# Performance work log

Measured on AMD Instinct MI355X. Metric: run time of the kernel, lower is better.

The kernel has to match this reference:

```python
import jax, jax.numpy as jnp
import numpy as np

B, N, L = 16, 128, 512            # batch, scan length, per-step feature (= configs.seq_len)
D, S, K, R, H = 1024, 16, 4, 64, 2048  # d_model, d_state, ker_size, dt_rank, hidden_dimention


def _mamba_params(key, scale=0.02):
    ks = jax.random.split(key, 6)
    return dict(
        in_w=jax.random.normal(ks[0], (2 * D, L)) * scale,
        conv_w=jax.random.normal(ks[1], (D, K)) * scale,
        conv_b=jnp.zeros((D,)),
        xproj_w=jax.random.normal(ks[2], (R + 2 * S, D)) * scale,
        dt_w=jax.random.normal(ks[3], (D, R)) * scale,
        dt_b=jax.random.normal(ks[4], (D,)) * scale,
        A_log=jnp.tile(jnp.log(jnp.arange(1, S + 1, dtype=jnp.float32)), (D, 1)),
        Dp=jnp.ones((D,)),
        out_w=jax.random.normal(ks[5], (L, D)) * scale,
    )


def setup_inputs():
    key = jax.random.key(0)
    kx, kf, kr, k1, k2 = jax.random.split(key, 5)
    inp = {"x": jax.random.normal(kx, (B, N, L), dtype=jnp.float32)}
    for pre, k in (("f_", kf), ("r_", kr)):
        for n, v in _mamba_params(k).items():
            inp[pre + n] = v
    inp["pu_w"] = jax.random.normal(k1, (H, L)) * 0.02
    inp["pu_b"] = jnp.zeros((H,))
    inp["pl_w"] = jax.random.normal(k2, (L, H)) * 0.02
    inp["pl_b"] = jnp.zeros((L,))
    inp["ln_g"] = jnp.ones((L,))
    inp["ln_b"] = jnp.zeros((L,))
    return inp


def _ln(x, g, b, eps=1e-5):
    m = x.mean(-1, keepdims=True)
    v = ((x - m) ** 2).mean(-1, keepdims=True)
    return (x - m) * jax.lax.rsqrt(v + eps) * g + b


def _dw_causal_conv(x, w, b):
    # x: [B,N,D]; depthwise causal conv along N with kernel [D,K]
    xt = jnp.pad(x.transpose(0, 2, 1), ((0, 0), (0, 0), (K - 1, 0)))  # [B,D,N+K-1]
    y = jax.lax.conv_general_dilated(xt, w[:, None, :], (1,), 'VALID',
                                     dimension_numbers=('NCH', 'OIH', 'NCH'),
                                     feature_group_count=D)
    return (y + b[None, :, None]).transpose(0, 2, 1)


def _mamba(x, in_w, conv_w, conv_b, xproj_w, dt_w, dt_b, A_log, Dp, out_w):
    # standard Mamba block (in_proj -> depthwise conv -> silu -> selective scan -> gate -> out_proj)
    xi, res = jnp.split(x @ in_w.T, 2, axis=-1)             # [B,N,D] each
    xc = jax.nn.silu(_dw_causal_conv(xi, conv_w, conv_b))   # [B,N,D]
    dbc = xc @ xproj_w.T                                    # [B,N,R+2S]
    dt, Bm, Cm = dbc[..., :R], dbc[..., R:R + S], dbc[..., R + S:]
    delta = jax.nn.softplus(dt @ dt_w.T + dt_b)             # [B,N,D]
    A = -jnp.exp(A_log)                                     # [D,S]
    dA = jnp.exp(delta[..., None] * A)                      # [B,N,D,S]
    dBx = delta[..., None] * Bm[:, :, None, :] * xc[..., None]

    def step(h, t):
        dA_t, dBx_t, C_t = t
        h = dA_t * h + dBx_t                                # [B,D,S]
        return h, jnp.einsum('bds,bs->bd', h, C_t)

    _, ys = jax.lax.scan(step, jnp.zeros((x.shape[0], D, S), x.dtype),
                         (dA.transpose(1, 0, 2, 3), dBx.transpose(1, 0, 2, 3), Cm.transpose(1, 0, 2)))
    y = ys.transpose(1, 0, 2) + xc * Dp                     # [B,N,D]
    y = y * jax.nn.silu(res)
    return y @ out_w.T                                      # [B,N,L]


def reference(x, f_in_w, f_conv_w, f_conv_b, f_xproj_w, f_dt_w, f_dt_b, f_A_log, f_Dp, f_out_w,
              r_in_w, r_conv_w, r_conv_b, r_xproj_w, r_dt_w, r_dt_b, r_A_log, r_Dp, r_out_w,
              pu_w, pu_b, pl_w, pl_b, ln_g, ln_b):
    y1 = _mamba(x, f_in_w, f_conv_w, f_conv_b, f_xproj_w, f_dt_w, f_dt_b, f_A_log, f_Dp, f_out_w)
    y2 = _mamba(x[:, ::-1, :], r_in_w, r_conv_w, r_conv_b, r_xproj_w, r_dt_w, r_dt_b, r_A_log, r_Dp, r_out_w)
    y3 = _ln(x + y1 + y2[:, ::-1, :], ln_g, ln_b)
    yp = jax.nn.relu(y3 @ pu_w.T + pu_b)
    yp = yp @ pl_w.T + pl_b
    return _ln(yp + y3, ln_g, ln_b)
```

## Files before the change

### kernel.cpp

```cpp
#include <hip/hip_runtime.h>
#include <hip/hip_bf16.h>
#include <cstdint>

typedef __hip_bfloat16 bf16;

constexpr int Bb = 16, Nn = 128, Ll = 512, Dd = 1024, Ss = 16, Rr = 64, Hh = 2048;
constexpr int Mm = Bb * Nn;
#define LOG2E 1.44269504088896340736f

using bf16x8 = __attribute__((ext_vector_type(8))) __bf16;
using bf16x4 = __attribute__((ext_vector_type(4))) __bf16;
using f32x4  = __attribute__((ext_vector_type(4))) float;

__device__ __forceinline__ float to_f(float x) { return x; }
__device__ __forceinline__ float to_f(bf16 x) { return __bfloat162float(x); }
__device__ __forceinline__ void store_t(float* p, float v) { *p = v; }
__device__ __forceinline__ void store_t(bf16* p, float v) { *p = __float2bfloat16(v); }
__device__ __forceinline__ __bf16 cvt1(float x) {
  bf16 h = __float2bfloat16(x);
  return *reinterpret_cast<__bf16*>(&h);
}
__device__ __forceinline__ float bfraw_to_f(__bf16 x) {
  bf16 h = *reinterpret_cast<bf16*>(&x);
  return __bfloat162float(h);
}
__device__ __forceinline__ bf16x8 load8(const bf16* p) { return *(const bf16x8*)p; }
__device__ __forceinline__ bf16x8 load8(const float* p) {
  float4 a = *(const float4*)p;
  float4 b = *(const float4*)(p + 4);
  bf16x8 r;
  r[0] = cvt1(a.x); r[1] = cvt1(a.y); r[2] = cvt1(a.z); r[3] = cvt1(a.w);
  r[4] = cvt1(b.x); r[5] = cvt1(b.y); r[6] = cvt1(b.z); r[7] = cvt1(b.w);
  return r;
}
__device__ __forceinline__ bf16x8 load8rt(const void* p, size_t idx, int isbf) {
  if (isbf) return load8((const bf16*)p + idx);
  return load8((const float*)p + idx);
}
__device__ __forceinline__ float ldf(const void* p, int i, int isbf) {
  if (isbf) return __bfloat162float(((const bf16*)p)[i]);
  return ((const float*)p)[i];
}
__device__ __forceinline__ void gld16(const bf16* g, __bf16* l) {
  __builtin_amdgcn_global_load_lds(
      (const __attribute__((address_space(1))) void*)g,
      (__attribute__((address_space(3))) void*)l, 16, 0, 0);
}
#if __has_builtin(__builtin_amdgcn_mov_dpp)
__device__ __forceinline__ float quad_xor1(float v) {
  int r = __builtin_amdgcn_mov_dpp(__builtin_bit_cast(int, v), 0xB1, 0xF, 0xF, true);
  return __builtin_bit_cast(float, r);
}
__device__ __forceinline__ float quad_xor2(float v) {
  int r = __builtin_amdgcn_mov_dpp(__builtin_bit_cast(int, v), 0x4E, 0xF, 0xF, true);
  return __builtin_bit_cast(float, r);
}
#else
__device__ __forceinline__ float quad_xor1(float v) { return __shfl_xor(v, 1, 64); }
__device__ __forceinline__ float quad_xor2(float v) { return __shfl_xor(v, 2, 64); }
#endif

enum { EPI_STORE = 0, EPI_BIAS_RELU = 1, EPI_ADD = 3, EPI_BIAS = 4, EPI_BIAS_SOFTPLUS = 5,
       EPI_ATOMIC = 6 };

__global__ void sniff_kernel(const unsigned short* __restrict__ xs, int* __restrict__ flags) {
  const int tid = threadIdx.x;
  int cnt = 0;
  for (int j = 0; j < 64; ++j) {
    int i = tid + j * 256;
    unsigned short u = xs[(size_t)i * 64];
    bf16 h = *reinterpret_cast<bf16*>(&u);
    float v = __bfloat162float(h);
    float a = fabsf(v);
    if (v == 0.f || (a > 0.0009765625f && a < 16.f)) ++cnt;
  }
  __shared__ int sc[256];
  sc[tid] = cnt;
  __syncthreads();
  for (int o = 128; o > 0; o >>= 1) {
    if (tid < o) sc[tid] += sc[tid + o];
    __syncthreads();
  }
  if (tid == 0) flags[0] = (sc[0] > 8192) ? 1 : 0;
}

__global__ __launch_bounds__(256) void prep_kernel(
    const int* __restrict__ flagp, const void* __restrict__ x,
    float* __restrict__ ZB, unsigned short* __restrict__ Xb,
    float* __restrict__ zerop,
    const void* __restrict__ fin, const void* __restrict__ rin,
    const void* __restrict__ fout, const void* __restrict__ rout,
    const void* __restrict__ puw, const void* __restrict__ plw,
    bf16* __restrict__ WBin, bf16* __restrict__ WBout,
    bf16* __restrict__ WBpu, bf16* __restrict__ WBpl) {
  const int isbf = *flagp;
  const int i = blockIdx.x * 256 + threadIdx.x;
  if (i < 262144) {
    float4 o;
    ushort4 u;
    if (isbf) {
      u = ((const ushort4*)x)[i];
      bf16 h0 = *reinterpret_cast<bf16*>(&u.x), h1 = *reinterpret_cast<bf16*>(&u.y);
      bf16 h2 = *reinterpret_cast<bf16*>(&u.z), h3 = *reinterpret_cast<bf16*>(&u.w);
      o = float4{__bfloat162float(h0), __bfloat162float(h1),
                 __bfloat162float(h2), __bfloat162float(h3)};
    } else {
      o = ((const float4*)x)[i];
      bf16 h0 = __float2bfloat16(o.x), h1 = __float2bfloat16(o.y);
      bf16 h2 = __float2bfloat16(o.z), h3 = __float2bfloat16(o.w);
      u = ushort4{*(unsigned short*)&h0, *(unsigned short*)&h1,
                  *(unsigned short*)&h2, *(unsigned short*)&h3};
    }
    ((float4*)ZB)[i] = o;
    ((ushort4*)Xb)[i] = u;
  } else if (i < 622592) {
    ((float4*)zerop)[i - 262144] = float4{0.f, 0.f, 0.f, 0.f};
  } else {
    const int j = i - 622592;
    const void* src;
    bf16* dst;
    int si;
    if (j < 131072) { src = fin; si = j; dst = WBin + (size_t)si * 8; }
    else if (j < 262144) { src = rin; si = j - 131072; dst = WBin + (size_t)1048576 + (size_t)si * 8; }
    else if (j < 393216) { src = puw; si = j - 262144; dst = WBpu + (size_t)si * 8; }
    else if (j < 524288) { src = plw; si = j - 393216; dst = WBpl + (size_t)si * 8; }
    else if (j < 589824) {
      src = fout; si = j - 524288;
      int e = si * 8;
      dst = WBout + (size_t)(e >> 10) * 2048 + (e & 1023);
    } else {
      src = rout; si = j - 589824;
      int e = si * 8;
      dst = WBout + (size_t)(e >> 10) * 2048 + 1024 + (e & 1023);
    }
    *(bf16x8*)dst = load8rt(src, (size_t)si * 8, isbf);
  }
}

constexpr int LDT2 = 72;

template <typename TC, int EPI>
__global__ __launch_bounds__(256) void gemm_rt(
    const int* __restrict__ flagp,
    const void* __restrict__ A, int lda, int abf,
    const void* __restrict__ Bw, const void* __restrict__ Bw2, int ldb,
    int bmode, int bsplit,
    TC* __restrict__ C, int ldc,
    const void* __restrict__ bias, const void* __restrict__ bias2,
    int N, int Kchunk, int zk, size_t a_doff, size_t c_doff) {
  const int isbf = *flagp;
  const int ab = (abf == 2) ? isbf : abf;
  __shared__ __align__(16) __bf16 As[64 * LDT2];
  __shared__ __align__(16) __bf16 Bs[64 * LDT2];
  const int tid = threadIdx.x;
  const int wave = tid >> 6, lane = tid & 63;
  const int quad = lane >> 4, l16 = lane & 15;
  const int wm = wave & 1, wn = wave >> 1;
  int bx = blockIdx.x, by = blockIdx.y;
  const int gx = gridDim.x, gy = gridDim.y;
  if ((gx & 7) == 0) {
    int id = bx + gx * by;
    int xcd = id & 7, sl = id >> 3;
    by = sl % gy;
    bx = (sl / gy) * 8 + xcd;
  }
  int zsl = blockIdx.z;
  const void* Ap = A;
  const void* Bp0 = Bw;
  const void* biasp = bias;
  if (bmode == 3) {
    const int dir = zsl / zk;
    zsl = zsl % zk;
    if (dir) {
      Ap = (const char*)A + a_doff * (size_t)(ab ? 2 : 4);
      C += c_doff;
      Bp0 = Bw2;
      biasp = bias2;
    }
  }
  const int m0 = by * 64, n0 = bx * 64;
  const int kb = zsl * Kchunk;
  const int srow = tid >> 3;
  const int scol = (tid & 7) * 8;
  f32x4 acc[2][2] = {};
  for (int k0 = kb; k0 < kb + Kchunk; k0 += 64) {
#pragma unroll
    for (int h = 0; h < 2; ++h) {
      int r = srow + h * 32;
      *(bf16x8*)(&As[r * LDT2 + scol]) =
          load8rt(Ap, (size_t)(m0 + r) * lda + k0 + scol, ab);
      int rb = n0 + r;
      rb = rb < N ? rb : N - 1;
      size_t bi = (size_t)rb * ldb + k0 + scol;
      *(bf16x8*)(&Bs[r * LDT2 + scol]) = load8rt(Bp0, bi, isbf);
    }
    __syncthreads();
#pragma unroll
    for (int kk2 = 0; kk2 < 2; ++kk2) {
      bf16x8 af[2], bfr[2];
#pragma unroll
      for (int i = 0; i < 2; ++i)
        af[i] = *(const bf16x8*)(&As[(wm * 32 + i * 16 + l16) * LDT2 + kk2 * 32 + quad * 8]);
#pragma unroll
      for (int j = 0; j < 2; ++j)
        bfr[j] = *(const bf16x8*)(&Bs[(wn * 32 + j * 16 + l16) * LDT2 + kk2 * 32 + quad * 8]);
#pragma unroll
      for (int i = 0; i < 2; ++i)
#pragma unroll
        for (int j = 0; j < 2; ++j)
          acc[i][j] = __builtin_amdgcn_mfma_f32_16x16x32_bf16(af[i], bfr[j], acc[i][j], 0, 0, 0);
    }
    __syncthreads();
  }
#pragma unroll
  for (int i = 0; i < 2; ++i) {
#pragma unroll
    for (int j = 0; j < 2; ++j) {
      const int col = n0 + wn * 32 + j * 16 + l16;
      if (col >= N) continue;
      float bv = 0.f;
      if (EPI == EPI_BIAS_RELU || EPI == EPI_BIAS || EPI == EPI_BIAS_SOFTPLUS)
        bv = ldf(biasp, col, isbf);
#pragma unroll
      for (int r = 0; r < 4; ++r) {
        const int row = m0 + wm * 32 + i * 16 + quad * 4 + r;
        size_t idx = (size_t)row * ldc + col;
        float v = acc[i][j][r];
        if (EPI == EPI_STORE) store_t(&C[idx], v);
        else if (EPI == EPI_BIAS_RELU) { v += bv; store_t(&C[idx], v > 0.f ? v : 0.f); }
        else if (EPI == EPI_BIAS) store_t(&C[idx], v + bv);
        else if (EPI == EPI_BIAS_SOFTPLUS) {
          v += bv;
          store_t(&C[idx], (v > 20.f) ? v : log1pf(__expf(v)));
        } else if (EPI == EPI_ATOMIC) {
          atomicAdd((float*)&C[idx], v);
        }
      }
    }
  }
}

template <typename TC, int EPI>
__global__ __launch_bounds__(256) void gemm128n(
    const int* __restrict__ flagp,
    const bf16* __restrict__ A, int lda,
    const bf16* __restrict__ Bw, int ldb,
    TC* __restrict__ C, int ldc,
    const void* __restrict__ bias,
    int Kchunk) {
  __shared__ __align__(16) __bf16 As[2][128 * 64];
  __shared__ __align__(16) __bf16 Bs[2][128 * 64];
  const int tid = threadIdx.x;
  const int wave = tid >> 6, lane = tid & 63;
  const int quad = lane >> 4, l16 = lane & 15;
  const int wr = wave >> 1, wc = wave & 1;
  int bx = blockIdx.x, by = blockIdx.y;
  const int gx = gridDim.x, gy = gridDim.y;
  if ((gx & 7) == 0) {
    int id = bx + gx * by;
    int xcd = id & 7, sl = id >> 3;
    by = sl % gy;
    bx = (sl / gy) * 8 + xcd;
  }
  const int m0 = by * 128, n0 = bx * 128;
  const int kb = blockIdx.z * Kchunk;
  const int kend = kb + Kchunk;
  const int lr = lane >> 3;
  const int lc = (lane & 7) * 8;
  auto STAGE = [&](int buf, int k0) {
#pragma unroll
    for (int rr = 0; rr < 4; ++rr) {
      const int rowb = rr * 32 + wave * 8;
      gld16(A + (size_t)(m0 + rowb + lr) * lda + k0 + lc, &As[buf][rowb * 64]);
      gld16(Bw + (size_t)(n0 + rowb + lr) * ldb + k0 + lc, &Bs[buf][rowb * 64]);
    }
  };
  f32x4 acc[4][4] = {};
  int cur = 0;
  STAGE(0, kb);
  __syncthreads();
  for (int k0 = kb; k0 < kend; k0 += 64) {
    if (k0 + 64 < kend) STAGE(cur ^ 1, k0 + 64);
#pragma unroll
    for (int kk = 0; kk < 2; ++kk) {
      bf16x8 af[4], bfr[4];
#pragma unroll
      for (int i = 0; i < 4; ++i)
        af[i] = *(const bf16x8*)(&As[cur][(wr * 64 + i * 16 + l16) * 64 + kk * 32 + quad * 8]);
#pragma unroll
      for (int j = 0; j < 4; ++j)
        bfr[j] = *(const bf16x8*)(&Bs[cur][(wc * 64 + j * 16 + l16) * 64 + kk * 32 + quad * 8]);
#pragma unroll
      for (int i = 0; i < 4; ++i)
#pragma unroll
        for (int j = 0; j < 4; ++j)
          acc[i][j] = __builtin_amdgcn_mfma_f32_16x16x32_bf16(af[i], bfr[j], acc[i][j], 0, 0, 0);
    }
    __syncthreads();
    cur ^= 1;
  }
  const int isbf = *flagp;
#pragma unroll
  for (int i = 0; i < 4; ++i) {
#pragma unroll
    for (int j = 0; j < 4; ++j) {
      const int col = n0 + wc * 64 + j * 16 + l16;
      float bv = 0.f;
      if (EPI == EPI_BIAS_RELU) bv = ldf(bias, col, isbf);
#pragma unroll
      for (int r = 0; r < 4; ++r) {
        const int row = m0 + wr * 64 + i * 16 + quad * 4 + r;
        size_t idx = (size_t)row * ldc + col;
        float v = acc[i][j][r];
        if (EPI == EPI_STORE) store_t(&C[idx], v);
        else if (EPI == EPI_BIAS_RELU) { v += bv; store_t(&C[idx], v > 0.f ? v : 0.f); }
        else if (EPI == EPI_ATOMIC) atomicAdd((float*)&C[idx], v);
      }
    }
  }
}

__global__ __launch_bounds__(256) void conv_silu_rt(
    const int* __restrict__ flagp, const bf16* __restrict__ X2b,
    const void* __restrict__ fcw, const void* __restrict__ fcb,
    const void* __restrict__ rcw, const void* __restrict__ rcb,
    bf16* __restrict__ XCb) {
  const int isbf = *flagp;
  const int dir = blockIdx.y >> 2;
  const int d = (blockIdx.y & 3) * 256 + threadIdx.x;
  const int m = blockIdx.x;
  const int t = m & (Nn - 1);
  const void* cw = dir ? rcw : fcw;
  const void* cb = dir ? rcb : fcb;
  float w0 = ldf(cw, d * 4 + 0, isbf), w1 = ldf(cw, d * 4 + 1, isbf);
  float w2 = ldf(cw, d * 4 + 2, isbf), w3 = ldf(cw, d * 4 + 3, isbf);
  float a = ldf(cb, d, isbf);
  const size_t base = (size_t)m * 4096 + (size_t)dir * 2048 + d;
  if (dir == 0) {
    if (t >= 3) a += w0 * to_f(X2b[base - 3 * 4096]);
    if (t >= 2) a += w1 * to_f(X2b[base - 2 * 4096]);
    if (t >= 1) a += w2 * to_f(X2b[base - 1 * 4096]);
    a += w3 * to_f(X2b[base]);
  } else {
    if (t + 3 < Nn) a += w0 * to_f(X2b[base + 3 * 4096]);
    if (t + 2 < Nn) a += w1 * to_f(X2b[base + 2 * 4096]);
    if (t + 1 < Nn) a += w2 * to_f(X2b[base + 1 * 4096]);
    a += w3 * to_f(X2b[base]);
  }
  const float s = a / (1.f + __builtin_amdgcn_exp2f(-a * LOG2E));
  XCb[(size_t)m * 2048 + (size_t)dir * 1024 + d] = __float2bfloat16(s);
}

__global__ __launch_bounds__(256) void scan_gate8(
    const int* __restrict__ flagp,
    const float* __restrict__ DBC0, bf16* __restrict__ XCb, const bf16* __restrict__ X2b,
    const bf16* __restrict__ DELTA0,
    const void* __restrict__ fAlog, const void* __restrict__ fDp,
    const void* __restrict__ rAlog, const void* __restrict__ rDp) {
  const int isbf = *flagp;
  const int dir = blockIdx.z;
  const float* DBC = DBC0 + (size_t)dir * Mm * 96;
  const bf16* DELTA = DELTA0 + (size_t)dir * Mm * 1024;
  const void* A_log = dir ? rAlog : fAlog;
  const void* Dp = dir ? rDp : fDp;
  __shared__ __align__(16) __bf16 sBC[Nn * 32];
  __shared__ __align__(16) __bf16 sD[Nn * 64];
  __shared__ __align__(16) __bf16 sX[Nn * 64];
  __shared__ __align__(16) __bf16 sG[Nn * 64];
  __shared__ __align__(16) __bf16 sY[Nn * 64];
  const int b = blockIdx.x;
  const int d0 = blockIdx.y * 64;
  const int tid = threadIdx.x;
  const size_t rowbase = (size_t)b * Nn;
  const size_t xc_col = (size_t)dir * 1024;
#pragma unroll
  for (int k = 0; k < 4; ++k) {
    int idx = tid + k * 256;
    int t = idx >> 3, c = idx & 7;
    float4 v = *(const float4*)(DBC + (rowbase + t) * 96 + 64 + c * 4);
    bf16x4 pv = {cvt1(v.x), cvt1(v.y), cvt1(v.z), cvt1(v.w)};
    int dst = (c < 4) ? (t * 32 + c * 8) : (t * 32 + (c - 4) * 8 + 4);
    *(bf16x4*)&sBC[dst] = pv;
  }
#pragma unroll
  for (int k = 0; k < 4; ++k) {
    int idx = tid + k * 256;
    int t = idx >> 3, h = idx & 7;
    *(uint4*)&sD[t * 64 + h * 8] =
        *(const uint4*)(DELTA + (rowbase + t) * 1024 + d0 + h * 8);
    *(uint4*)&sX[t * 64 + h * 8] =
        *(const uint4*)(XCb + (rowbase + t) * 2048 + xc_col + d0 + h * 8);
    bf16x8 rv = *(const bf16x8*)(X2b + (rowbase + t) * 4096 + (size_t)dir * 2048 + 1024 + d0 + h * 8);
    bf16x8 gv;
#pragma unroll
    for (int e = 0; e < 8; ++e) {
      float r = bfraw_to_f(rv[e]);
      gv[e] = cvt1(r / (1.f + __builtin_amdgcn_exp2f(-r * LOG2E)));
    }
    *(bf16x8*)&sG[t * 64 + h * 8] = gv;
  }
  __syncthreads();
  const int wv = tid >> 6, lane = tid & 63;
  const int sg = lane & 3, dl = lane >> 2;
  const int d_local = wv * 16 + dl;
  const int d = d0 + d_local;
  float A_[4];
#pragma unroll
  for (int j = 0; j < 4; ++j)
    A_[j] = -__expf(ldf(A_log, d * Ss + sg * 4 + j, isbf)) * LOG2E;
  const float dp = ldf(Dp, d, isbf);
  float h0 = 0.f, h1 = 0.f, h2 = 0.f, h3 = 0.f;
  for (int pg = 0; pg < Nn / 4; ++pg) {
    float accs[4], xvs[4];
#pragma unroll
    for (int u = 0; u < 4; ++u) {
      const int p = pg * 4 + u;
      const int t = dir ? (Nn - 1 - p) : p;
      const float dv = bfraw_to_f(sD[t * 64 + d_local]);
      const float xv = bfraw_to_f(sX[t * 64 + d_local]);
      bf16x8 bc = *(const bf16x8*)&sBC[t * 32 + sg * 8];
      const float dx = dv * xv;
      h0 = __builtin_amdgcn_exp2f(dv * A_[0]) * h0 + dx * bfraw_to_f(bc[0]);
      h1 = __builtin_amdgcn_exp2f(dv * A_[1]) * h1 + dx * bfraw_to_f(bc[1]);
      h2 = __builtin_amdgcn_exp2f(dv * A_[2]) * h2 + dx * bfraw_to_f(bc[2]);
      h3 = __builtin_amdgcn_exp2f(dv * A_[3]) * h3 + dx * bfraw_to_f(bc[3]);
      accs[u] = h0 * bfraw_to_f(bc[4]) + h1 * bfraw_to_f(bc[5]) +
                h2 * bfraw_to_f(bc[6]) + h3 * bfraw_to_f(bc[7]);
      xvs[u] = xv;
    }
#pragma unroll
    for (int u = 0; u < 4; ++u) {
      float a = accs[u];
      a += quad_xor1(a);
      a += quad_xor2(a);
      if (sg == 0) {
        const int p = pg * 4 + u;
        const int t = dir ? (Nn - 1 - p) : p;
        const float g = bfraw_to_f(sG[t * 64 + d_local]);
        sY[t * 64 + d_local] = cvt1((a + xvs[u] * dp) * g);
      }
    }
  }
  __syncthreads();
#pragma unroll
  for (int k = 0; k < 4; ++k) {
    int idx = tid + k * 256;
    int t = idx >> 3, h = idx & 7;
    *(uint4*)(XCb + (rowbase + t) * 2048 + xc_col + d0 + h * 8) =
        *(const uint4*)&sY[t * 64 + h * 8];
  }
}

template <int MODE>
__global__ __launch_bounds__(256) void ln_rt(const int* __restrict__ flagp,
                                             const float* __restrict__ Z,
                                             const float* __restrict__ Zadd,
                                             const void* __restrict__ g,
                                             const void* __restrict__ bb,
                                             const void* __restrict__ pb,
                                             void* __restrict__ outp,
                                             bf16* __restrict__ outp2) {
  const int isbf = *flagp;
  const int row = blockIdx.x;
  const int tid = threadIdx.x;
  const int c0 = tid * 2;
  const float2* z = (const float2*)(Z + (size_t)row * Ll);
  float2 v = z[tid];
  if (MODE == 1) {
    const float2* za = (const float2*)(Zadd + (size_t)row * Ll);
    float2 a = za[tid];
    v.x += a.x + ldf(pb, c0, isbf);
    v.y += a.y + ldf(pb, c0 + 1, isbf);
  }
  float s = v.x + v.y, q = v.x * v.x + v.y * v.y;
#pragma unroll
  for (int o = 32; o > 0; o >>= 1) {
    s += __shfl_xor(s, o, 64);
    q += __shfl_xor(q, o, 64);
  }
  __shared__ float ss[4], qq[4];
  const int wv = tid >> 6, ln = tid & 63;
  if (ln == 0) { ss[wv] = s; qq[wv] = q; }
  __syncthreads();
  s = ss[0] + ss[1] + ss[2] + ss[3];
  q = qq[0] + qq[1] + qq[2] + qq[3];
  const float mean = s * (1.f / Ll);
  const float var = q * (1.f / Ll) - mean * mean;
  const float rs = rsqrtf(var + 1e-5f);
  const float o0 = (v.x - mean) * rs * ldf(g, c0, isbf) + ldf(bb, c0, isbf);
  const float o1 = (v.y - mean) * rs * ldf(g, c0 + 1, isbf) + ldf(bb, c0 + 1, isbf);
  if (MODE == 0) {
    float* out = (float*)outp;
    out[(size_t)row * Ll + c0] = o0;
    out[(size_t)row * Ll + c0 + 1] = o1;
    outp2[(size_t)row * Ll + c0] = __float2bfloat16(o0);
    outp2[(size_t)row * Ll + c0 + 1] = __float2bfloat16(o1);
  } else {
    if (isbf) {
      bf16* out = (bf16*)outp;
      out[(size_t)row * Ll + c0] = __float2bfloat16(o0);
      out[(size_t)row * Ll + c0 + 1] = __float2bfloat16(o1);
    } else {
      float* out = (float*)outp;
      out[(size_t)row * Ll + c0] = o0;
      out[(size_t)row * Ll + c0 + 1] = o1;
    }
  }
}

extern "C" void kernel_launch(void* const* d_in, const int* in_sizes, int n_in, void* d_out,
                              int out_size, void* d_ws, size_t ws_size, hipStream_t stream) {
  char* ws = (char*)d_ws;
  int* flags = (int*)ws;
  bf16* X2b = (bf16*)(ws + 256);
  bf16* XCb = X2b + (size_t)Mm * 4096;
  bf16* Y3b = XCb + (size_t)Mm * 2048;
  bf16* DELTA = Y3b + (size_t)Mm * 512;
  bf16* Xb = DELTA + (size_t)2 * Mm * 1024;
  bf16* WBin = Xb + (size_t)Mm * 512;
  bf16* WBout = WBin + (size_t)4096 * 512;
  bf16* WBpu = WBout + (size_t)512 * 2048;
  bf16* WBpl = WBpu + (size_t)2048 * 512;
  float* DBC = (float*)(WBpl + (size_t)512 * 2048);
  float* Z2 = DBC + (size_t)2 * Mm * 96;
  float* ZB = Z2 + (size_t)Mm * 512;
  float* Y3 = ZB + (size_t)Mm * 512;
  bf16* H1 = X2b;
  size_t needed = 256 +
                  2 * ((size_t)Mm * 4096 + (size_t)Mm * 2048 + (size_t)Mm * 512 +
                       (size_t)2 * Mm * 1024 + (size_t)Mm * 512 +
                       (size_t)4096 * 512 + (size_t)512 * 2048 +
                       (size_t)2048 * 512 + (size_t)512 * 2048) +
                  4 * ((size_t)2 * Mm * 96 + (size_t)3 * Mm * 512);
  if (ws_size < needed) return;

  const void* x = d_in[0];
  const dim3 blk(256);

  sniff_kernel<<<dim3(1), blk, 0, stream>>>((const unsigned short*)x, flags);
  prep_kernel<<<dim3(4992), blk, 0, stream>>>(
      flags, x, ZB, (unsigned short*)Xb, DBC,
      d_in[1], d_in[10], d_in[9], d_in[18], d_in[19], d_in[21],
      WBin, WBout, WBpu, WBpl);
  gemm128n<bf16, EPI_STORE><<<dim3(32, 16), blk, 0, stream>>>(
      flags, Xb, Ll, WBin, Ll, X2b, 4096, nullptr, Ll);
  conv_silu_rt<<<dim3(Mm, 8), blk, 0, stream>>>(flags, X2b, d_in[2], d_in[3],
                                                d_in[11], d_in[12], XCb);
  gemm_rt<float, EPI_ATOMIC><<<dim3(2, 32, 8), blk, 0, stream>>>(
      flags, XCb, 2048, 1, d_in[4], d_in[13], Dd, 3, 0,
      DBC, 96, nullptr, nullptr, 96, 256, 4, 1024, (size_t)Mm * 96);
  gemm_rt<bf16, EPI_BIAS_SOFTPLUS><<<dim3(16, 32, 2), blk, 0, stream>>>(
      flags, DBC, 96, 0, d_in[5], d_in[14], Rr, 3, 0,
      DELTA, 1024, d_in[6], d_in[15], 1024, Rr, 1, (size_t)Mm * 96, (size_t)Mm * 1024);
  scan_gate8<<<dim3(Bb, Dd / 64, 2), blk, 0, stream>>>(
      flags, DBC, XCb, X2b, DELTA, d_in[7], d_in[8], d_in[16], d_in[17]);
  gemm128n<float, EPI_ATOMIC><<<dim3(4, 16, 4), blk, 0, stream>>>(
      flags, XCb, 2048, WBout, 2048, ZB, Ll, nullptr, Ll);
  ln_rt<0><<<dim3(Mm), blk, 0, stream>>>(flags, ZB, nullptr, d_in[23], d_in[24], nullptr,
                                         (void*)Y3, Y3b);
  gemm128n<bf16, EPI_BIAS_RELU><<<dim3(16, 16), blk, 0, stream>>>(
      flags, Y3b, Ll, WBpu, Ll, H1, Hh, d_in[20], Ll);
  gemm128n<float, EPI_ATOMIC><<<dim3(4, 16, 4), blk, 0, stream>>>(
      flags, H1, Hh, WBpl, 2048, Z2, Ll, nullptr, Ll);
  ln_rt<1><<<dim3(Mm), blk, 0, stream>>>(flags, Z2, Y3, d_in[23], d_in[24], d_in[22],
                                         d_out, nullptr);

  (void)in_sizes; (void)n_in; (void)out_size;
}
```

Measured before the change: 314.2 us.

## Fuse dt projection and softplus into scan kernel via MFMA

Removes the separate dt-projection GEMM launch and the DELTA global buffer. Each scan block now computes its 128x64 delta tile in place with MFMA, reading the DBC dt columns and dt weights, then applies bias and softplus into shared memory. The gate and output tiles reuse the staging shared memory to keep the LDS footprint the same. This saves a launch and the DELTA write and read, at the cost of extra per-block compute and an added sync phase in front of the scan.

Result: no change. 312.4 us (median of 2 runs) (-0.6%).

```diff
diff --git a/kernel.cpp b/kernel.cpp
--- a/kernel.cpp
+++ b/kernel.cpp
@@ -351,28 +351,43 @@
   XCb[(size_t)m * 2048 + (size_t)dir * 1024 + d] = __float2bfloat16(s);
 }
 
-__global__ __launch_bounds__(256) void scan_gate8(
+__global__ __launch_bounds__(256) void scan_gate9(
     const int* __restrict__ flagp,
     const float* __restrict__ DBC0, bf16* __restrict__ XCb, const bf16* __restrict__ X2b,
-    const bf16* __restrict__ DELTA0,
+    const void* __restrict__ fdtw, const void* __restrict__ fdtb,
+    const void* __restrict__ rdtw, const void* __restrict__ rdtb,
     const void* __restrict__ fAlog, const void* __restrict__ fDp,
     const void* __restrict__ rAlog, const void* __restrict__ rDp) {
   const int isbf = *flagp;
   const int dir = blockIdx.z;
   const float* DBC = DBC0 + (size_t)dir * Mm * 96;
-  const bf16* DELTA = DELTA0 + (size_t)dir * Mm * 1024;
+  const void* dtw = dir ? rdtw : fdtw;
+  const void* dtb = dir ? rdtb : fdtb;
   const void* A_log = dir ? rAlog : fAlog;
   const void* Dp = dir ? rDp : fDp;
   __shared__ __align__(16) __bf16 sBC[Nn * 32];
   __shared__ __align__(16) __bf16 sD[Nn * 64];
   __shared__ __align__(16) __bf16 sX[Nn * 64];
-  __shared__ __align__(16) __bf16 sG[Nn * 64];
-  __shared__ __align__(16) __bf16 sY[Nn * 64];
+  __shared__ __align__(16) __bf16 uni[2 * Nn * 64];
+  __bf16* At = uni;
+  __bf16* Bt = uni + 128 * LDT2;
+  __bf16* sG = uni;
+  __bf16* sY = uni + Nn * 64;
   const int b = blockIdx.x;
   const int d0 = blockIdx.y * 64;
   const int tid = threadIdx.x;
   const size_t rowbase = (size_t)b * Nn;
   const size_t xc_col = (size_t)dir * 1024;
+  const int wave = tid >> 6, lane = tid & 63;
+  const int quad = lane >> 4, l16 = lane & 15;
+#pragma unroll
+  for (int k = 0; k < 8; ++k) {
+    int idx = tid + k * 256;
+    int t = idx >> 4, c4 = (idx & 15) * 4;
+    float4 v = *(const float4*)(DBC + (rowbase + t) * 96 + c4);
+    bf16x4 pv = {cvt1(v.x), cvt1(v.y), cvt1(v.z), cvt1(v.w)};
+    *(bf16x4*)&At[t * LDT2 + c4] = pv;
+  }
 #pragma unroll
   for (int k = 0; k < 4; ++k) {
     int idx = tid + k * 256;
@@ -383,13 +398,57 @@
     *(bf16x4*)&sBC[dst] = pv;
   }
 #pragma unroll
+  for (int k = 0; k < 2; ++k) {
+    int c8 = tid + k * 256;
+    int n = c8 >> 3, r8 = (c8 & 7) * 8;
+    *(bf16x8*)&Bt[n * LDT2 + r8] = load8rt(dtw, (size_t)(d0 + n) * Rr + r8, isbf);
+  }
+#pragma unroll
   for (int k = 0; k < 4; ++k) {
     int idx = tid + k * 256;
     int t = idx >> 3, h = idx & 7;
-    *(uint4*)&sD[t * 64 + h * 8] =
-        *(const uint4*)(DELTA + (rowbase + t) * 1024 + d0 + h * 8);
     *(uint4*)&sX[t * 64 + h * 8] =
         *(const uint4*)(XCb + (rowbase + t) * 2048 + xc_col + d0 + h * 8);
+  }
+  __syncthreads();
+  {
+    f32x4 dacc[2][4] = {};
+#pragma unroll
+    for (int kk = 0; kk < 2; ++kk) {
+      bf16x8 af[2], bf_[4];
+#pragma unroll
+      for (int i = 0; i < 2; ++i)
+        af[i] = *(const bf16x8*)(&At[(wave * 32 + i * 16 + l16) * LDT2 + kk * 32 + quad * 8]);
+#pragma unroll
+      for (int j = 0; j < 4; ++j)
+        bf_[j] = *(const bf16x8*)(&Bt[(j * 16 + l16) * LDT2 + kk * 32 + quad * 8]);
+#pragma unroll
+      for (int i = 0; i < 2; ++i)
+#pragma unroll
+        for (int j = 0; j < 4; ++j)
+          dacc[i][j] = __builtin_amdgcn_mfma_f32_16x16x32_bf16(af[i], bf_[j], dacc[i][j], 0, 0, 0);
+    }
+#pragma unroll
+    for (int i = 0; i < 2; ++i) {
+#pragma unroll
+      for (int j = 0; j < 4; ++j) {
+        const int col = j * 16 + l16;
+        const float bv = ldf(dtb, d0 + col, isbf);
+#pragma unroll
+        for (int r = 0; r < 4; ++r) {
+          const int row = wave * 32 + i * 16 + quad * 4 + r;
+          float v = dacc[i][j][r] + bv;
+          v = (v > 20.f) ? v : log1pf(__expf(v));
+          sD[row * 64 + col] = cvt1(v);
+        }
+      }
+    }
+  }
+  __syncthreads();
+#pragma unroll
+  for (int k = 0; k < 4; ++k) {
+    int idx = tid + k * 256;
+    int t = idx >> 3, h = idx & 7;
     bf16x8 rv = *(const bf16x8*)(X2b + (rowbase + t) * 4096 + (size_t)dir * 2048 + 1024 + d0 + h * 8);
     bf16x8 gv;
 #pragma unroll
@@ -400,7 +459,7 @@
     *(bf16x8*)&sG[t * 64 + h * 8] = gv;
   }
   __syncthreads();
-  const int wv = tid >> 6, lane = tid & 63;
+  const int wv = wave;
   const int sg = lane & 3, dl = lane >> 2;
   const int d_local = wv * 16 + dl;
   const int d = d0 + d_local;
@@ -515,8 +574,7 @@
   bf16* X2b = (bf16*)(ws + 256);
   bf16* XCb = X2b + (size_t)Mm * 4096;
   bf16* Y3b = XCb + (size_t)Mm * 2048;
-  bf16* DELTA = Y3b + (size_t)Mm * 512;
-  bf16* Xb = DELTA + (size_t)2 * Mm * 1024;
+  bf16* Xb = Y3b + (size_t)Mm * 512;
   bf16* WBin = Xb + (size_t)Mm * 512;
   bf16* WBout = WBin + (size_t)4096 * 512;
   bf16* WBpu = WBout + (size_t)512 * 2048;
@@ -527,8 +585,7 @@
   float* Y3 = ZB + (size_t)Mm * 512;
   bf16* H1 = X2b;
   size_t needed = 256 +
-                  2 * ((size_t)Mm * 4096 + (size_t)Mm * 2048 + (size_t)Mm * 512 +
-                       (size_t)2 * Mm * 1024 + (size_t)Mm * 512 +
+                  2 * ((size_t)Mm * 4096 + (size_t)Mm * 2048 + (size_t)2 * Mm * 512 +
                        (size_t)4096 * 512 + (size_t)512 * 2048 +
                        (size_t)2048 * 512 + (size_t)512 * 2048) +
                   4 * ((size_t)2 * Mm * 96 + (size_t)3 * Mm * 512);
@@ -549,11 +606,9 @@
   gemm_rt<float, EPI_ATOMIC><<<dim3(2, 32, 8), blk, 0, stream>>>(
       flags, XCb, 2048, 1, d_in[4], d_in[13], Dd, 3, 0,
       DBC, 96, nullptr, nullptr, 96, 256, 4, 1024, (size_t)Mm * 96);
-  gemm_rt<bf16, EPI_BIAS_SOFTPLUS><<<dim3(16, 32, 2), blk, 0, stream>>>(
-      flags, DBC, 96, 0, d_in[5], d_in[14], Rr, 3, 0,
-      DELTA, 1024, d_in[6], d_in[15], 1024, Rr, 1, (size_t)Mm * 96, (size_t)Mm * 1024);
-  scan_gate8<<<dim3(Bb, Dd / 64, 2), blk, 0, stream>>>(
-      flags, DBC, XCb, X2b, DELTA, d_in[7], d_in[8], d_in[16], d_in[17]);
+  scan_gate9<<<dim3(Bb, Dd / 64, 2), blk, 0, stream>>>(
+      flags, DBC, XCb, X2b, d_in[5], d_in[6], d_in[14], d_in[15],
+      d_in[7], d_in[8], d_in[16], d_in[17]);
   gemm128n<float, EPI_ATOMIC><<<dim3(4, 16, 4), blk, 0, stream>>>(
       flags, XCb, 2048, WBout, 2048, ZB, Ll, nullptr, Ll);
   ln_rt<0><<<dim3(Mm), blk, 0, stream>>>(flags, ZB, nullptr, d_in[23], d_in[24], nullptr,
```
